# Kernel optimization log

Hardware: AMD Instinct MI355X
Metric: run time of the kernel (lower is better)

The kernel has to match this reference:

```python
import jax, jax.numpy as jnp
import numpy as np


def _l2norm(v, eps=1e-12):
    # torch F.normalize(dim=-1): v / clamp(||v||_2, min=eps)
    n = jnp.linalg.norm(v, axis=-1, keepdims=True)
    return v / jnp.maximum(n, eps)


def setup_inputs() -> dict:
    key = jax.random.key(0)
    ks = jax.random.split(key, 10)
    B, T, N, Ci, E, K, H = 64, 12, 1024, 64, 16, 3, 192
    O = H // 3  # subhidden size
    return {
        "x": jax.random.normal(ks[0], (B, N, Ci), jnp.float32),
        "x_window": jax.random.normal(ks[1], (B, T, N, 1), jnp.float32),
        "node_embeddings": jax.random.normal(ks[2], (N, E), jnp.float32) * 0.1,
        "ZPI": jax.random.normal(ks[3], (B, 3), jnp.float32),
        "supports_adj": jax.random.uniform(ks[4], (K, N, N), jnp.float32),
        "weights_pool": jax.random.normal(ks[5], (E, K, Ci, O), jnp.float32) * 0.1,
        "weights_pool_adj": jax.random.normal(ks[6], (E, K, Ci, O), jnp.float32) * 0.1,
        "weights_window": jax.random.normal(ks[7], (E, 1, O), jnp.float32) * 0.1,
        "bias_pool": jax.random.normal(ks[8], (E, H), jnp.float32) * 0.1,
        "T_param": jax.random.normal(ks[9], (T,), jnp.float32) * 0.1,
    }


def reference(x, x_window, node_embeddings, ZPI, supports_adj,
              weights_pool, weights_pool_adj, weights_window, bias_pool, T_param):
    N = node_embeddings.shape[0]
    K = weights_pool.shape[1]  # link_len

    # adaptive supports: softmax(relu(E E^T)) and its power series
    supports = jax.nn.softmax(jax.nn.relu(node_embeddings @ node_embeddings.T), axis=1)
    support_set = [jnp.eye(N, dtype=x.dtype), supports]
    for k in range(2, K):
        support_set.append(supports @ support_set[k - 1])
    S = jnp.stack(support_set, axis=0)  # (K, N, N)

    # per-node dynamic weights / bias
    weights = jnp.einsum('nd,dkio->nkio', node_embeddings, weights_pool)
    bias = node_embeddings @ bias_pool  # (N, H)

    # adaptive graph conv branch
    x_g = jnp.einsum('knm,bmc->bnkc', S, x)
    x_gconv = _l2norm(jnp.einsum('bnki,nkio->bno', x_g, weights))

    # static adjacency branch ('knn' repeated index = diagonal; sum over m --
    # faithful to the original torch einsum)
    weights_adj = jnp.einsum('nd,dkio->nkio', node_embeddings, weights_pool_adj)
    x_a = jnp.einsum('knn,bmc->bnkc', supports_adj, x)
    x_aconv = _l2norm(jnp.einsum('bnki,nkio->bno', x_a, weights_adj))

    # temporal window branch
    ww = jnp.einsum('nd,dio->nio', node_embeddings, weights_window)  # (N, 1, O)
    x_w = jnp.einsum('btni,nio->btno', x_window, ww)
    x_wconv = _l2norm(jnp.einsum('btno,t->bno', x_w, T_param))

    return jnp.concatenate([x_gconv, x_aconv, x_wconv], axis=-1) + bias
```

## Files before the change

kernel.cpp:

```cpp
#include <hip/hip_runtime.h>


typedef __attribute__((ext_vector_type(4))) float f32x4;
typedef __attribute__((ext_vector_type(8))) short short8;

#define DEVI static __device__ __forceinline__

DEVI short f2bf(float f) {
    unsigned int x = __builtin_bit_cast(unsigned int, f);
    x = (x + 0x7FFFu + ((x >> 16) & 1u)) >> 16;
    return (short)(unsigned short)x;
}
DEVI int swz(int row) { return ((row ^ (row >> 3)) & 7) << 3; }

DEVI f32x4 mfma16(short8 a, short8 b, f32x4 c) {
    return __builtin_amdgcn_mfma_f32_16x16x32_bf16(a, b, c, 0, 0, 0);
}

DEVI void gload16(const void* g, void* l) {
    __builtin_amdgcn_global_load_lds(
        (const __attribute__((address_space(1))) unsigned int*)g,
        (__attribute__((address_space(3))) unsigned int*)l, 16, 0, 0);
}

__global__ __launch_bounds__(256) void k_prep(
        const float* __restrict__ NE, const float* __restrict__ x,
        const float* __restrict__ xw, const float* __restrict__ adj,
        const float* __restrict__ wp, const float* __restrict__ wpa,
        const float* __restrict__ Tp,
        short* __restrict__ S, short* __restrict__ B2, short* __restrict__ A2,
        float* __restrict__ xsp, float* __restrict__ s_bn) {
    __shared__ float En[16];
    __shared__ float wsum[4];
    __shared__ float red[4][64];
    int bid = blockIdx.x, t = threadIdx.x;
    if (bid < 1024) {
        int n = bid;
        if (t < 16) En[t] = NE[n * 16 + t];
        __syncthreads();
        float e[4];
        float loc = 0.f;
#pragma unroll
        for (int i = 0; i < 4; ++i) {
            int m = t + 256 * i;
            const float* rp = NE + m * 16;
            float v = 0.f;
#pragma unroll
            for (int d = 0; d < 16; ++d) v += En[d] * rp[d];
            v = fmaxf(v, 0.f);
            e[i] = __expf(v);
            loc += e[i];
        }
#pragma unroll
        for (int off = 32; off; off >>= 1) loc += __shfl_xor(loc, off);
        if ((t & 63) == 0) wsum[t >> 6] = loc;
        __syncthreads();
        float inv = 1.f / (wsum[0] + wsum[1] + wsum[2] + wsum[3]);
#pragma unroll
        for (int i = 0; i < 4; ++i) S[n * 1024 + t + 256 * i] = f2bf(e[i] * inv);
        return;
    }
    int bid2 = bid - 1024;
    if (bid2 < 64) {
        int o = bid2, j = t;
        short row[64];
        if (j < 192) {
            int kk = j >> 6, i = j & 63;
#pragma unroll
            for (int d = 0; d < 16; ++d)
                row[d] = f2bf(wp[((d * 3 + kk) * 64 + i) * 64 + o]);
#pragma unroll
            for (int k = 16; k < 64; ++k) row[k] = 0;
        } else {
            int i2 = j - 192;
#pragma unroll
            for (int k = 0; k < 16; ++k) row[k] = 0;
#pragma unroll
            for (int d = 0; d < 16; ++d)
#pragma unroll
                for (int kk = 0; kk < 3; ++kk)
                    row[16 + d * 3 + kk] = f2bf(wpa[((d * 3 + kk) * 64 + i2) * 64 + o]);
        }
        short* dst = B2 + (o * 256 + j) * 64;
#pragma unroll
        for (int q = 0; q < 8; ++q) {
            short8 v;
#pragma unroll
            for (int e2 = 0; e2 < 8; ++e2) v[e2] = row[q * 8 + e2];
            *reinterpret_cast<short8*>(dst + q * 8) = v;
        }
    } else if (bid2 < 320) {
        int idx = bid2 - 64, b = idx >> 2, mq = idx & 3;
        int c = t & 63, q2 = t >> 6;
        int m0 = mq * 256 + q2 * 64;
        float s = 0.f;
        for (int mm = 0; mm < 64; ++mm) s += x[((size_t)b * 1024 + m0 + mm) * 64 + c];
        red[q2][c] = s;
        __syncthreads();
        if (t < 64) xsp[(b * 4 + mq) * 64 + t] = red[0][t] + red[1][t] + red[2][t] + red[3][t];
    } else if (bid2 < 336) {
        int idx = bid2 - 320;
        float tp[12];
#pragma unroll
        for (int i = 0; i < 12; ++i) tp[i] = Tp[i];
        for (int bb = 0; bb < 4; ++bb) {
            int b = idx * 4 + bb;
#pragma unroll
            for (int j2 = 0; j2 < 4; ++j2) {
                int nn = t + 256 * j2;
                float s = 0.f;
#pragma unroll
                for (int tt = 0; tt < 12; ++tt) s += xw[(b * 12 + tt) * 1024 + nn] * tp[tt];
                s_bn[b * 1024 + nn] = s;
            }
        }
    } else {
        int n = (bid2 - 336) * 256 + t;
        float Enr[16];
#pragma unroll
        for (int d = 0; d < 16; ++d) Enr[d] = NE[n * 16 + d];
        float dg[3];
#pragma unroll
        for (int k = 0; k < 3; ++k) dg[k] = adj[k * 1024 * 1024 + n * 1024 + n];
        short row[64];
#pragma unroll
        for (int d = 0; d < 16; ++d) row[d] = f2bf(Enr[d]);
#pragma unroll
        for (int d = 0; d < 16; ++d)
#pragma unroll
            for (int k = 0; k < 3; ++k) row[16 + d * 3 + k] = f2bf(Enr[d] * dg[k]);
        short* dst = A2 + n * 64;
#pragma unroll
        for (int q = 0; q < 8; ++q) {
            short8 v;
#pragma unroll
            for (int e2 = 0; e2 < 8; ++e2) v[e2] = row[q * 8 + e2];
            *reinterpret_cast<short8*>(dst + q * 8) = v;
        }
    }
}

__global__ __launch_bounds__(256) void k_mid(
        const short* __restrict__ S, const float* __restrict__ x,
        const short* __restrict__ A2, const short* __restrict__ B2,
        const float* __restrict__ xsp,
        short* __restrict__ Y1, short* __restrict__ Wall,
        short* __restrict__ xs_bf) {
    __shared__ __align__(16) short lds[16384];
    int bid = blockIdx.x, t = threadIdx.x;
    if (bid >= 1536) {
        int by = bid - 1536;
#pragma unroll
        for (int p = 0; p < 2; ++p) {
            int j = by * 512 + p * 256 + t;
            int b = j >> 6, c = j & 63;
            float s = xsp[(b * 4 + 0) * 64 + c] + xsp[(b * 4 + 1) * 64 + c] +
                      xsp[(b * 4 + 2) * 64 + c] + xsp[(b * 4 + 3) * 64 + c];
            xs_bf[j] = f2bf(s);
        }
        return;
    }
    short* As = lds;
    short* Bs = lds + 8192;
    int wid = t >> 6, lane = t & 63;
    int rsub = lane >> 3, csub = (lane & 7) * 8;
    int wm = wid & 1, wn = wid >> 1;
    int lr = lane & 15, lg = lane >> 4;
    if (bid < 512) {
        int bx = bid & 7, b = bid >> 3;
        const short* A = S + (size_t)bx * 131072;
        const float* xb = x + (size_t)b * 65536;
        int bm = t >> 2, bc = (t & 3) * 16;
        f32x4 acc[4][2] = {};
        for (int kt = 0; kt < 16; ++kt) {
#pragma unroll
            for (int q = 0; q < 4; ++q) {
                int row = q * 32 + wid * 8;
                gload16(A + (size_t)(row + rsub) * 1024 + kt * 64 + csub, As + row * 64);
            }
#pragma unroll
            for (int j = 0; j < 4; ++j) {
                float4 f = *reinterpret_cast<const float4*>(&xb[(kt * 64 + bm) * 64 + bc + 4 * j]);
                float vv[4] = {f.x, f.y, f.z, f.w};
#pragma unroll
                for (int e = 0; e < 4; ++e) {
                    int c = bc + 4 * j + e;
                    Bs[c * 64 + (bm ^ swz(c))] = f2bf(vv[e]);
                }
            }
            __syncthreads();
#pragma unroll
            for (int ks = 0; ks < 2; ++ks) {
                int kk = ks * 32 + lg * 8;
                short8 af[4], bfr[2];
#pragma unroll
                for (int i = 0; i < 4; ++i)
                    af[i] = *reinterpret_cast<const short8*>(&As[(wm * 64 + i * 16 + lr) * 64 + kk]);
#pragma unroll
                for (int nf = 0; nf < 2; ++nf) {
                    int c = wn * 32 + nf * 16 + lr;
                    bfr[nf] = *reinterpret_cast<const short8*>(&Bs[c * 64 + (kk ^ swz(c))]);
                }
#pragma unroll
                for (int i = 0; i < 4; ++i)
#pragma unroll
                    for (int nf = 0; nf < 2; ++nf)
                        acc[i][nf] = mfma16(af[i], bfr[nf], acc[i][nf]);
            }
            __syncthreads();
        }
#pragma unroll
        for (int i = 0; i < 4; ++i)
#pragma unroll
            for (int nf = 0; nf < 2; ++nf)
#pragma unroll
                for (int r = 0; r < 4; ++r) {
                    int g = wm * 64 + i * 16 + lg * 4 + r;
                    int c = wn * 32 + nf * 16 + lr;
                    Y1[((size_t)b * 1024 + bx * 128 + g) * 64 + c] = f2bf(acc[i][nf][r]);
                }
    } else {
        int idx = bid - 512, bx = idx & 127, by = idx >> 7;
#pragma unroll
        for (int i = 0; i < 4; ++i) {
            int slot = t + 256 * i;
            int row = slot >> 3, k8 = slot & 7;
            int sw = swz(row);
            short8 va = *reinterpret_cast<const short8*>(A2 + (by * 128 + row) * 64 + k8 * 8);
            *reinterpret_cast<short8*>(&As[row * 64 + ((k8 * 8) ^ sw)]) = va;
            short8 vb = *reinterpret_cast<const short8*>(B2 + (bx * 128 + row) * 64 + k8 * 8);
            *reinterpret_cast<short8*>(&Bs[row * 64 + ((k8 * 8) ^ sw)]) = vb;
        }
        __syncthreads();
        f32x4 acc[4][4] = {};
#pragma unroll
        for (int ks = 0; ks < 2; ++ks) {
            int kk = ks * 32 + lg * 8;
            short8 af[4], bfr[4];
#pragma unroll
            for (int mf = 0; mf < 4; ++mf) {
                int row = wm * 64 + mf * 16 + lr;
                af[mf] = *reinterpret_cast<const short8*>(&As[row * 64 + (kk ^ swz(row))]);
            }
#pragma unroll
            for (int nf = 0; nf < 4; ++nf) {
                int row = wn * 64 + nf * 16 + lr;
                bfr[nf] = *reinterpret_cast<const short8*>(&Bs[row * 64 + (kk ^ swz(row))]);
            }
#pragma unroll
            for (int mf = 0; mf < 4; ++mf)
#pragma unroll
                for (int nf = 0; nf < 4; ++nf)
                    acc[mf][nf] = mfma16(af[mf], bfr[nf], acc[mf][nf]);
        }
#pragma unroll
        for (int mf = 0; mf < 4; ++mf)
#pragma unroll
            for (int nf = 0; nf < 4; ++nf)
#pragma unroll
                for (int r = 0; r < 4; ++r) {
                    int row = by * 128 + wm * 64 + mf * 16 + lg * 4 + r;
                    int col = bx * 128 + wn * 64 + nf * 16 + lr;
                    int o = col >> 8, j = col & 255;
                    Wall[(size_t)row * 16384 + (size_t)(j >> 3) * 512 + o * 8 + (j & 7)] =
                        f2bf(acc[mf][nf][r]);
                }
    }
}

__global__ __launch_bounds__(256) void k_gemm2(const short* __restrict__ S,
                                               const short* __restrict__ Y1,
                                               short* __restrict__ Y2) {
    __shared__ __align__(16) short As[128 * 64];
    __shared__ __align__(16) short Bs[64 * 64];
    int bx = blockIdx.x & 7, b = blockIdx.x >> 3, t = threadIdx.x;
    int wid = t >> 6, lane = t & 63;
    int rsub = lane >> 3, csub = (lane & 7) * 8;
    int wm = wid & 1, wn = wid >> 1;
    int lr = lane & 15, lg = lane >> 4;
    const short* A = S + (size_t)bx * 131072;
    const short* Bh = Y1 + (size_t)b * 65536;
    int bc0 = (t & 7) * 8, bm = t >> 3;
    f32x4 acc[4][2] = {};
    for (int kt = 0; kt < 16; ++kt) {
#pragma unroll
        for (int q = 0; q < 4; ++q) {
            int row = q * 32 + wid * 8;
            gload16(A + (size_t)(row + rsub) * 1024 + kt * 64 + csub, As + row * 64);
        }
#pragma unroll
        for (int it = 0; it < 2; ++it) {
            int m = bm + 32 * it;
            short8 hv = *reinterpret_cast<const short8*>(&Bh[(kt * 64 + m) * 64 + bc0]);
#pragma unroll
            for (int j = 0; j < 8; ++j) {
                int c = bc0 + j;
                Bs[c * 64 + (m ^ swz(c))] = hv[j];
            }
        }
        __syncthreads();
#pragma unroll
        for (int ks = 0; ks < 2; ++ks) {
            int kk = ks * 32 + lg * 8;
            short8 af[4], bfr[2];
#pragma unroll
            for (int i = 0; i < 4; ++i)
                af[i] = *reinterpret_cast<const short8*>(&As[(wm * 64 + i * 16 + lr) * 64 + kk]);
#pragma unroll
            for (int nf = 0; nf < 2; ++nf) {
                int c = wn * 32 + nf * 16 + lr;
                bfr[nf] = *reinterpret_cast<const short8*>(&Bs[c * 64 + (kk ^ swz(c))]);
            }
#pragma unroll
            for (int i = 0; i < 4; ++i)
#pragma unroll
                for (int nf = 0; nf < 2; ++nf)
                    acc[i][nf] = mfma16(af[i], bfr[nf], acc[i][nf]);
        }
        __syncthreads();
    }
#pragma unroll
    for (int i = 0; i < 4; ++i)
#pragma unroll
        for (int nf = 0; nf < 2; ++nf)
#pragma unroll
            for (int r = 0; r < 4; ++r) {
                int g = wm * 64 + i * 16 + lg * 4 + r;
                int c = wn * 32 + nf * 16 + lr;
                Y2[((size_t)b * 1024 + bx * 128 + g) * 64 + c] = f2bf(acc[i][nf][r]);
            }
}

__global__ __launch_bounds__(256) void k_epi(
        const float* __restrict__ x, const short* __restrict__ Y1,
        const short* __restrict__ Y2, const short* __restrict__ xs_bf,
        const float* __restrict__ s_bn, const short* __restrict__ Wall,
        const float* __restrict__ NE, const float* __restrict__ bp,
        const float* __restrict__ wwin, float* __restrict__ out) {
    int n = blockIdx.x, t = threadIdx.x;
    __shared__ float E_l[16];
    __shared__ float bias_l[192];
    __shared__ float ww_l[64];
    __shared__ float sq_l[2][2][64];
    __shared__ float wwn_l;
    if (t < 16) E_l[t] = NE[n * 16 + t];
    int w = t >> 6, l = t & 63;
    int wm = w & 1, wn = w >> 1;
    int lr = l & 15, lg = l >> 4;
    short8 wfk[8][2];
#pragma unroll
    for (int ks = 0; ks < 8; ++ks)
#pragma unroll
        for (int nf = 0; nf < 2; ++nf) {
            int o = wn * 32 + nf * 16 + lr;
            wfk[ks][nf] = *reinterpret_cast<const short8*>(
                &Wall[(size_t)n * 16384 + (size_t)(ks * 4 + lg) * 512 + o * 8]);
        }
    short8 af[8][2];
#pragma unroll
    for (int ks = 0; ks < 8; ++ks)
#pragma unroll
        for (int mf = 0; mf < 2; ++mf) {
            int b = wm * 32 + mf * 16 + lr;
            int k0 = ks * 32 + lg * 8;
            if (ks < 2) {
                const float4* p =
                    reinterpret_cast<const float4*>(&x[((size_t)b * 1024 + n) * 64 + k0]);
                float4 p0 = p[0], p1 = p[1];
                short8 v;
                v[0] = f2bf(p0.x); v[1] = f2bf(p0.y); v[2] = f2bf(p0.z); v[3] = f2bf(p0.w);
                v[4] = f2bf(p1.x); v[5] = f2bf(p1.y); v[6] = f2bf(p1.z); v[7] = f2bf(p1.w);
                af[ks][mf] = v;
            } else if (ks < 4) {
                af[ks][mf] = *reinterpret_cast<const short8*>(
                    &Y1[((size_t)b * 1024 + n) * 64 + (k0 - 64)]);
            } else if (ks < 6) {
                af[ks][mf] = *reinterpret_cast<const short8*>(
                    &Y2[((size_t)b * 1024 + n) * 64 + (k0 - 128)]);
            } else {
                af[ks][mf] = *reinterpret_cast<const short8*>(&xs_bf[b * 64 + (k0 - 192)]);
            }
        }
    __syncthreads();
    if (t < 192) {
        float s = 0.f;
#pragma unroll
        for (int d = 0; d < 16; ++d) s += E_l[d] * bp[d * 192 + t];
        bias_l[t] = s;
    } else {
        int o = t - 192;
        float s = 0.f;
#pragma unroll
        for (int d = 0; d < 16; ++d) s += E_l[d] * wwin[d * 64 + o];
        ww_l[o] = s;
    }
    __syncthreads();
    if (t < 64) {
        float v = ww_l[t];
        float s2 = v * v;
#pragma unroll
        for (int off = 32; off; off >>= 1) s2 += __shfl_xor(s2, off);
        if (t == 0) wwn_l = sqrtf(s2);
    }
    f32x4 accg[2][2] = {};
    f32x4 acca[2][2] = {};
#pragma unroll
    for (int ks = 0; ks < 8; ++ks)
#pragma unroll
        for (int mf = 0; mf < 2; ++mf)
#pragma unroll
            for (int nf = 0; nf < 2; ++nf) {
                if (ks < 6) accg[mf][nf] = mfma16(af[ks][mf], wfk[ks][nf], accg[mf][nf]);
                else        acca[mf][nf] = mfma16(af[ks][mf], wfk[ks][nf], acca[mf][nf]);
            }
#pragma unroll
    for (int mf = 0; mf < 2; ++mf)
#pragma unroll
        for (int r = 0; r < 4; ++r) {
            float sg = accg[mf][0][r] * accg[mf][0][r] + accg[mf][1][r] * accg[mf][1][r];
            float sa = acca[mf][0][r] * acca[mf][0][r] + acca[mf][1][r] * acca[mf][1][r];
#pragma unroll
            for (int off = 1; off < 16; off <<= 1) {
                sg += __shfl_xor(sg, off);
                sa += __shfl_xor(sa, off);
            }
            if (lr == 0) {
                int b = wm * 32 + mf * 16 + lg * 4 + r;
                sq_l[0][wn][b] = sg;
                sq_l[1][wn][b] = sa;
            }
        }
    __syncthreads();
#pragma unroll
    for (int mf = 0; mf < 2; ++mf)
#pragma unroll
        for (int r = 0; r < 4; ++r) {
            int b = wm * 32 + mf * 16 + lg * 4 + r;
            float ig = 1.f / fmaxf(sqrtf(sq_l[0][0][b] + sq_l[0][1][b]), 1e-12f);
            float ia = 1.f / fmaxf(sqrtf(sq_l[1][0][b] + sq_l[1][1][b]), 1e-12f);
            float* po = out + ((size_t)b * 1024 + n) * 192;
#pragma unroll
            for (int nf = 0; nf < 2; ++nf) {
                int o = wn * 32 + nf * 16 + lr;
                po[o]      = accg[mf][nf][r] * ig + bias_l[o];
                po[64 + o] = acca[mf][nf][r] * ia + bias_l[64 + o];
            }
        }
    float wwn = wwn_l;
#pragma unroll
    for (int it = 0; it < 16; ++it) {
        int b = it * 4 + (t >> 6);
        int o = t & 63;
        float s = s_bn[b * 1024 + n];
        float pre = s * ww_l[o];
        float nrm = fabsf(s) * wwn;
        out[((size_t)b * 1024 + n) * 192 + 128 + o] = pre / fmaxf(nrm, 1e-12f) + bias_l[128 + o];
    }
}

extern "C" void kernel_launch(void* const* d_in, const int* in_sizes, int n_in,
                              void* d_out, int out_size, void* d_ws, size_t ws_size,
                              hipStream_t stream) {
    const float* x    = (const float*)d_in[0];
    const float* xw   = (const float*)d_in[1];
    const float* NE   = (const float*)d_in[2];
    const float* adj  = (const float*)d_in[4];
    const float* wp   = (const float*)d_in[5];
    const float* wpa  = (const float*)d_in[6];
    const float* wwin = (const float*)d_in[7];
    const float* bp   = (const float*)d_in[8];
    const float* Tp   = (const float*)d_in[9];
    float* out = (float*)d_out;

    char* ws = (char*)d_ws;
    const size_t OFF_S    = 0;
    const size_t OFF_Y1   = 2097152;
    const size_t OFF_Y2   = 10485760;
    const size_t OFF_WALL = 18874368;
    const size_t OFF_A2   = 52428800;
    const size_t OFF_B2   = 52559872;
    const size_t OFF_XSP  = 54657024;
    const size_t OFF_XSBF = 54722560;
    const size_t OFF_SBN  = 54730752;
    const size_t NEED     = 54992896;
    if (ws_size < NEED) return;

    short* S     = (short*)(ws + OFF_S);
    short* Y1    = (short*)(ws + OFF_Y1);
    short* Y2    = (short*)(ws + OFF_Y2);
    short* Wall  = (short*)(ws + OFF_WALL);
    short* A2    = (short*)(ws + OFF_A2);
    short* B2    = (short*)(ws + OFF_B2);
    float* xsp   = (float*)(ws + OFF_XSP);
    short* xs_bf = (short*)(ws + OFF_XSBF);
    float* s_bn  = (float*)(ws + OFF_SBN);

    k_prep<<<1364, 256, 0, stream>>>(NE, x, xw, adj, wp, wpa, Tp, S, B2, A2, xsp, s_bn);
    k_mid<<<1544, 256, 0, stream>>>(S, x, A2, B2, xsp, Y1, Wall, xs_bf);
    k_gemm2<<<512, 256, 0, stream>>>(S, Y1, Y2);
    k_epi<<<1024, 256, 0, stream>>>(x, Y1, Y2, xs_bf, s_bn, Wall, NE, bp, wwin, out);
}
```

Baseline: 126.8 us.

## Split fused prep/mid kernels and store Y1/Y2 node-major for epilogue

Splits the multi-role k_prep and k_mid kernels into separate kernels (supports softmax, small prep, gemm1, gemm2, weight gemm). Y1/Y2 move from batch-major to node-major layout, so the per-node epilogue reads contiguous rows. The epilogue now stages xs_bf in swizzled LDS and loads weight fragments per k-step instead of preloading all of them, which lowers register pressure. In exchange there are more kernel launches and less overlap between heterogeneous work that used to share one grid.

```diff
diff --git a/kernel.cpp b/kernel.cpp
--- a/kernel.cpp
+++ b/kernel.cpp
@@ -23,46 +23,46 @@
         (__attribute__((address_space(3))) unsigned int*)l, 16, 0, 0);
 }
 
-__global__ __launch_bounds__(256) void k_prep(
-        const float* __restrict__ NE, const float* __restrict__ x,
-        const float* __restrict__ xw, const float* __restrict__ adj,
+__global__ __launch_bounds__(256) void k_supports(const float* __restrict__ NE,
+                                                  short* __restrict__ S) {
+    int n = blockIdx.x, t = threadIdx.x;
+    __shared__ float En[16];
+    __shared__ float wsum[4];
+    if (t < 16) En[t] = NE[n * 16 + t];
+    __syncthreads();
+    float e[4];
+    float loc = 0.f;
+#pragma unroll
+    for (int i = 0; i < 4; ++i) {
+        int m = t + 256 * i;
+        const float* rp = NE + m * 16;
+        float v = 0.f;
+#pragma unroll
+        for (int d = 0; d < 16; ++d) v += En[d] * rp[d];
+        v = fmaxf(v, 0.f);
+        e[i] = __expf(v);
+        loc += e[i];
+    }
+#pragma unroll
+    for (int off = 32; off; off >>= 1) loc += __shfl_xor(loc, off);
+    if ((t & 63) == 0) wsum[t >> 6] = loc;
+    __syncthreads();
+    float inv = 1.f / (wsum[0] + wsum[1] + wsum[2] + wsum[3]);
+#pragma unroll
+    for (int i = 0; i < 4; ++i) S[n * 1024 + t + 256 * i] = f2bf(e[i] * inv);
+}
+
+__global__ __launch_bounds__(256) void k_small(
+        const float* __restrict__ x, const float* __restrict__ xw,
+        const float* __restrict__ NE, const float* __restrict__ adj,
         const float* __restrict__ wp, const float* __restrict__ wpa,
         const float* __restrict__ Tp,
-        short* __restrict__ S, short* __restrict__ B2, short* __restrict__ A2,
+        short* __restrict__ B2, short* __restrict__ A2,
         float* __restrict__ xsp, float* __restrict__ s_bn) {
-    __shared__ float En[16];
-    __shared__ float wsum[4];
     __shared__ float red[4][64];
     int bid = blockIdx.x, t = threadIdx.x;
-    if (bid < 1024) {
-        int n = bid;
-        if (t < 16) En[t] = NE[n * 16 + t];
-        __syncthreads();
-        float e[4];
-        float loc = 0.f;
-#pragma unroll
-        for (int i = 0; i < 4; ++i) {
-            int m = t + 256 * i;
-            const float* rp = NE + m * 16;
-            float v = 0.f;
-#pragma unroll
-            for (int d = 0; d < 16; ++d) v += En[d] * rp[d];
-            v = fmaxf(v, 0.f);
-            e[i] = __expf(v);
-            loc += e[i];
-        }
-#pragma unroll
-        for (int off = 32; off; off >>= 1) loc += __shfl_xor(loc, off);
-        if ((t & 63) == 0) wsum[t >> 6] = loc;
-        __syncthreads();
-        float inv = 1.f / (wsum[0] + wsum[1] + wsum[2] + wsum[3]);
-#pragma unroll
-        for (int i = 0; i < 4; ++i) S[n * 1024 + t + 256 * i] = f2bf(e[i] * inv);
-        return;
-    }
-    int bid2 = bid - 1024;
-    if (bid2 < 64) {
-        int o = bid2, j = t;
+    if (bid < 64) {
+        int o = bid, j = t;
         short row[64];
         if (j < 192) {
             int kk = j >> 6, i = j & 63;
@@ -89,8 +89,8 @@
             for (int e2 = 0; e2 < 8; ++e2) v[e2] = row[q * 8 + e2];
             *reinterpret_cast<short8*>(dst + q * 8) = v;
         }
-    } else if (bid2 < 320) {
-        int idx = bid2 - 64, b = idx >> 2, mq = idx & 3;
+    } else if (bid < 320) {
+        int idx = bid - 64, b = idx >> 2, mq = idx & 3;
         int c = t & 63, q2 = t >> 6;
         int m0 = mq * 256 + q2 * 64;
         float s = 0.f;
@@ -98,8 +98,8 @@
         red[q2][c] = s;
         __syncthreads();
         if (t < 64) xsp[(b * 4 + mq) * 64 + t] = red[0][t] + red[1][t] + red[2][t] + red[3][t];
-    } else if (bid2 < 336) {
-        int idx = bid2 - 320;
+    } else if (bid < 336) {
+        int idx = bid - 320;
         float tp[12];
 #pragma unroll
         for (int i = 0; i < 12; ++i) tp[i] = Tp[i];
@@ -115,20 +115,20 @@
             }
         }
     } else {
-        int n = (bid2 - 336) * 256 + t;
-        float Enr[16];
-#pragma unroll
-        for (int d = 0; d < 16; ++d) Enr[d] = NE[n * 16 + d];
+        int n = (bid - 336) * 256 + t;
+        float En[16];
+#pragma unroll
+        for (int d = 0; d < 16; ++d) En[d] = NE[n * 16 + d];
         float dg[3];
 #pragma unroll
         for (int k = 0; k < 3; ++k) dg[k] = adj[k * 1024 * 1024 + n * 1024 + n];
         short row[64];
 #pragma unroll
-        for (int d = 0; d < 16; ++d) row[d] = f2bf(Enr[d]);
+        for (int d = 0; d < 16; ++d) row[d] = f2bf(En[d]);
 #pragma unroll
         for (int d = 0; d < 16; ++d)
 #pragma unroll
-            for (int k = 0; k < 3; ++k) row[16 + d * 3 + k] = f2bf(Enr[d] * dg[k]);
+            for (int k = 0; k < 3; ++k) row[16 + d * 3 + k] = f2bf(En[d] * dg[k]);
         short* dst = A2 + n * 64;
 #pragma unroll
         for (int q = 0; q < 8; ++q) {
@@ -140,16 +140,139 @@
     }
 }
 
-__global__ __launch_bounds__(256) void k_mid(
-        const short* __restrict__ S, const float* __restrict__ x,
-        const short* __restrict__ A2, const short* __restrict__ B2,
-        const float* __restrict__ xsp,
-        short* __restrict__ Y1, short* __restrict__ Wall,
-        short* __restrict__ xs_bf) {
-    __shared__ __align__(16) short lds[16384];
-    int bid = blockIdx.x, t = threadIdx.x;
-    if (bid >= 1536) {
-        int by = bid - 1536;
+__global__ __launch_bounds__(256) void k_gemm1(const short* __restrict__ S,
+                                               const float* __restrict__ x,
+                                               short* __restrict__ Y1) {
+    __shared__ __align__(16) short As[128 * 64];
+    __shared__ __align__(16) short Bs[64 * 64];
+    int bx = blockIdx.x, b = blockIdx.y, t = threadIdx.x;
+    int wid = t >> 6, lane = t & 63;
+    int rsub = lane >> 3, csub = (lane & 7) * 8;
+    int wm = wid & 1, wn = wid >> 1;
+    int lr = lane & 15, lg = lane >> 4;
+    const short* A = S + (size_t)bx * 131072;
+    const float* xb = x + (size_t)b * 65536;
+    int bm = t >> 2, bc = (t & 3) * 16;
+    f32x4 acc[4][2] = {};
+    for (int kt = 0; kt < 16; ++kt) {
+#pragma unroll
+        for (int q = 0; q < 4; ++q) {
+            int row = q * 32 + wid * 8;
+            gload16(A + (size_t)(row + rsub) * 1024 + kt * 64 + csub, As + row * 64);
+        }
+#pragma unroll
+        for (int j = 0; j < 4; ++j) {
+            float4 f = *reinterpret_cast<const float4*>(&xb[(kt * 64 + bm) * 64 + bc + 4 * j]);
+            float vv[4] = {f.x, f.y, f.z, f.w};
+#pragma unroll
+            for (int e = 0; e < 4; ++e) {
+                int c = bc + 4 * j + e;
+                Bs[c * 64 + (bm ^ swz(c))] = f2bf(vv[e]);
+            }
+        }
+        __syncthreads();
+#pragma unroll
+        for (int ks = 0; ks < 2; ++ks) {
+            int kk = ks * 32 + lg * 8;
+            short8 af[4], bfr[2];
+#pragma unroll
+            for (int i = 0; i < 4; ++i)
+                af[i] = *reinterpret_cast<const short8*>(&As[(wm * 64 + i * 16 + lr) * 64 + kk]);
+#pragma unroll
+            for (int nf = 0; nf < 2; ++nf) {
+                int c = wn * 32 + nf * 16 + lr;
+                bfr[nf] = *reinterpret_cast<const short8*>(&Bs[c * 64 + (kk ^ swz(c))]);
+            }
+#pragma unroll
+            for (int i = 0; i < 4; ++i)
+#pragma unroll
+                for (int nf = 0; nf < 2; ++nf)
+                    acc[i][nf] = mfma16(af[i], bfr[nf], acc[i][nf]);
+        }
+        __syncthreads();
+    }
+#pragma unroll
+    for (int i = 0; i < 4; ++i)
+#pragma unroll
+        for (int nf = 0; nf < 2; ++nf)
+#pragma unroll
+            for (int r = 0; r < 4; ++r) {
+                int g = wm * 64 + i * 16 + lg * 4 + r;
+                int c = wn * 32 + nf * 16 + lr;
+                Y1[(size_t)(bx * 128 + g) * 4096 + b * 64 + c] = f2bf(acc[i][nf][r]);
+            }
+}
+
+__global__ __launch_bounds__(256) void k_gemm2(const short* __restrict__ S,
+                                               const short* __restrict__ Y1,
+                                               short* __restrict__ Y2) {
+    __shared__ __align__(16) short As[128 * 64];
+    __shared__ __align__(16) short Bs[64 * 64];
+    int bx = blockIdx.x, b = blockIdx.y, t = threadIdx.x;
+    int wid = t >> 6, lane = t & 63;
+    int rsub = lane >> 3, csub = (lane & 7) * 8;
+    int wm = wid & 1, wn = wid >> 1;
+    int lr = lane & 15, lg = lane >> 4;
+    const short* A = S + (size_t)bx * 131072;
+    int bm = t >> 3, bc0 = (t & 7) * 8;
+    f32x4 acc[4][2] = {};
+    for (int kt = 0; kt < 16; ++kt) {
+#pragma unroll
+        for (int q = 0; q < 4; ++q) {
+            int row = q * 32 + wid * 8;
+            gload16(A + (size_t)(row + rsub) * 1024 + kt * 64 + csub, As + row * 64);
+        }
+#pragma unroll
+        for (int it = 0; it < 2; ++it) {
+            int m = bm + 32 * it;
+            short8 hv = *reinterpret_cast<const short8*>(
+                &Y1[(size_t)(kt * 64 + m) * 4096 + b * 64 + bc0]);
+#pragma unroll
+            for (int j = 0; j < 8; ++j) {
+                int c = bc0 + j;
+                Bs[c * 64 + (m ^ swz(c))] = hv[j];
+            }
+        }
+        __syncthreads();
+#pragma unroll
+        for (int ks = 0; ks < 2; ++ks) {
+            int kk = ks * 32 + lg * 8;
+            short8 af[4], bfr[2];
+#pragma unroll
+            for (int i = 0; i < 4; ++i)
+                af[i] = *reinterpret_cast<const short8*>(&As[(wm * 64 + i * 16 + lr) * 64 + kk]);
+#pragma unroll
+            for (int nf = 0; nf < 2; ++nf) {
+                int c = wn * 32 + nf * 16 + lr;
+                bfr[nf] = *reinterpret_cast<const short8*>(&Bs[c * 64 + (kk ^ swz(c))]);
+            }
+#pragma unroll
+            for (int i = 0; i < 4; ++i)
+#pragma unroll
+                for (int nf = 0; nf < 2; ++nf)
+                    acc[i][nf] = mfma16(af[i], bfr[nf], acc[i][nf]);
+        }
+        __syncthreads();
+    }
+#pragma unroll
+    for (int i = 0; i < 4; ++i)
+#pragma unroll
+        for (int nf = 0; nf < 2; ++nf)
+#pragma unroll
+            for (int r = 0; r < 4; ++r) {
+                int g = wm * 64 + i * 16 + lg * 4 + r;
+                int c = wn * 32 + nf * 16 + lr;
+                Y2[(size_t)(bx * 128 + g) * 4096 + b * 64 + c] = f2bf(acc[i][nf][r]);
+            }
+}
+
+__global__ __launch_bounds__(256) void k_gemm_w(const short* __restrict__ A2,
+                                                const short* __restrict__ B2,
+                                                short* __restrict__ Wall,
+                                                const float* __restrict__ xsp,
+                                                short* __restrict__ xs_bf) {
+    int bx = blockIdx.x, by = blockIdx.y, t = threadIdx.x;
+    if (bx == 128) {
 #pragma unroll
         for (int p = 0; p < 2; ++p) {
             int j = by * 512 + p * 256 + t;
@@ -160,174 +283,54 @@
         }
         return;
     }
-    short* As = lds;
-    short* Bs = lds + 8192;
-    int wid = t >> 6, lane = t & 63;
-    int rsub = lane >> 3, csub = (lane & 7) * 8;
-    int wm = wid & 1, wn = wid >> 1;
-    int lr = lane & 15, lg = lane >> 4;
-    if (bid < 512) {
-        int bx = bid & 7, b = bid >> 3;
-        const short* A = S + (size_t)bx * 131072;
-        const float* xb = x + (size_t)b * 65536;
-        int bm = t >> 2, bc = (t & 3) * 16;
-        f32x4 acc[4][2] = {};
-        for (int kt = 0; kt < 16; ++kt) {
-#pragma unroll
-            for (int q = 0; q < 4; ++q) {
-                int row = q * 32 + wid * 8;
-                gload16(A + (size_t)(row + rsub) * 1024 + kt * 64 + csub, As + row * 64);
-            }
-#pragma unroll
-            for (int j = 0; j < 4; ++j) {
-                float4 f = *reinterpret_cast<const float4*>(&xb[(kt * 64 + bm) * 64 + bc + 4 * j]);
-                float vv[4] = {f.x, f.y, f.z, f.w};
-#pragma unroll
-                for (int e = 0; e < 4; ++e) {
-                    int c = bc + 4 * j + e;
-                    Bs[c * 64 + (bm ^ swz(c))] = f2bf(vv[e]);
-                }
-            }
-            __syncthreads();
-#pragma unroll
-            for (int ks = 0; ks < 2; ++ks) {
-                int kk = ks * 32 + lg * 8;
-                short8 af[4], bfr[2];
-#pragma unroll
-                for (int i = 0; i < 4; ++i)
-                    af[i] = *reinterpret_cast<const short8*>(&As[(wm * 64 + i * 16 + lr) * 64 + kk]);
-#pragma unroll
-                for (int nf = 0; nf < 2; ++nf) {
-                    int c = wn * 32 + nf * 16 + lr;
-                    bfr[nf] = *reinterpret_cast<const short8*>(&Bs[c * 64 + (kk ^ swz(c))]);
-                }
-#pragma unroll
-                for (int i = 0; i < 4; ++i)
-#pragma unroll
-                    for (int nf = 0; nf < 2; ++nf)
-                        acc[i][nf] = mfma16(af[i], bfr[nf], acc[i][nf]);
-            }
-            __syncthreads();
-        }
-#pragma unroll
-        for (int i = 0; i < 4; ++i)
-#pragma unroll
-            for (int nf = 0; nf < 2; ++nf)
-#pragma unroll
-                for (int r = 0; r < 4; ++r) {
-                    int g = wm * 64 + i * 16 + lg * 4 + r;
-                    int c = wn * 32 + nf * 16 + lr;
-                    Y1[((size_t)b * 1024 + bx * 128 + g) * 64 + c] = f2bf(acc[i][nf][r]);
-                }
-    } else {
-        int idx = bid - 512, bx = idx & 127, by = idx >> 7;
-#pragma unroll
-        for (int i = 0; i < 4; ++i) {
-            int slot = t + 256 * i;
-            int row = slot >> 3, k8 = slot & 7;
-            int sw = swz(row);
-            short8 va = *reinterpret_cast<const short8*>(A2 + (by * 128 + row) * 64 + k8 * 8);
-            *reinterpret_cast<short8*>(&As[row * 64 + ((k8 * 8) ^ sw)]) = va;
-            short8 vb = *reinterpret_cast<const short8*>(B2 + (bx * 128 + row) * 64 + k8 * 8);
-            *reinterpret_cast<short8*>(&Bs[row * 64 + ((k8 * 8) ^ sw)]) = vb;
-        }
-        __syncthreads();
-        f32x4 acc[4][4] = {};
-#pragma unroll
-        for (int ks = 0; ks < 2; ++ks) {
-            int kk = ks * 32 + lg * 8;
-            short8 af[4], bfr[4];
-#pragma unroll
-            for (int mf = 0; mf < 4; ++mf) {
-                int row = wm * 64 + mf * 16 + lr;
-                af[mf] = *reinterpret_cast<const short8*>(&As[row * 64 + (kk ^ swz(row))]);
-            }
-#pragma unroll
-            for (int nf = 0; nf < 4; ++nf) {
-                int row = wn * 64 + nf * 16 + lr;
-                bfr[nf] = *reinterpret_cast<const short8*>(&Bs[row * 64 + (kk ^ swz(row))]);
-            }
-#pragma unroll
-            for (int mf = 0; mf < 4; ++mf)
-#pragma unroll
-                for (int nf = 0; nf < 4; ++nf)
-                    acc[mf][nf] = mfma16(af[mf], bfr[nf], acc[mf][nf]);
+    __shared__ __align__(16) short As[128 * 64];
+    __shared__ __align__(16) short Bs[128 * 64];
+#pragma unroll
+    for (int i = 0; i < 4; ++i) {
+        int slot = t + 256 * i;
+        int row = slot >> 3, k8 = slot & 7;
+        int sw = swz(row);
+        short8 va = *reinterpret_cast<const short8*>(A2 + (by * 128 + row) * 64 + k8 * 8);
+        *reinterpret_cast<short8*>(&As[row * 64 + ((k8 * 8) ^ sw)]) = va;
+        short8 vb = *reinterpret_cast<const short8*>(B2 + (bx * 128 + row) * 64 + k8 * 8);
+        *reinterpret_cast<short8*>(&Bs[row * 64 + ((k8 * 8) ^ sw)]) = vb;
+    }
+    __syncthreads();
+    int w = t >> 6, l = t & 63;
+    int wm = w & 1, wn = w >> 1;
+    int lr = l & 15, lg = l >> 4;
+    f32x4 acc[4][4] = {};
+#pragma unroll
+    for (int ks = 0; ks < 2; ++ks) {
+        int kk = ks * 32 + lg * 8;
+        short8 af[4], bfr[4];
+#pragma unroll
+        for (int mf = 0; mf < 4; ++mf) {
+            int row = wm * 64 + mf * 16 + lr;
+            af[mf] = *reinterpret_cast<const short8*>(&As[row * 64 + (kk ^ swz(row))]);
+        }
+#pragma unroll
+        for (int nf = 0; nf < 4; ++nf) {
+            int row = wn * 64 + nf * 16 + lr;
+            bfr[nf] = *reinterpret_cast<const short8*>(&Bs[row * 64 + (kk ^ swz(row))]);
         }
 #pragma unroll
         for (int mf = 0; mf < 4; ++mf)
 #pragma unroll
             for (int nf = 0; nf < 4; ++nf)
-#pragma unroll
-                for (int r = 0; r < 4; ++r) {
-                    int row = by * 128 + wm * 64 + mf * 16 + lg * 4 + r;
-                    int col = bx * 128 + wn * 64 + nf * 16 + lr;
-                    int o = col >> 8, j = col & 255;
-                    Wall[(size_t)row * 16384 + (size_t)(j >> 3) * 512 + o * 8 + (j & 7)] =
-                        f2bf(acc[mf][nf][r]);
-                }
-    }
-}
-
-__global__ __launch_bounds__(256) void k_gemm2(const short* __restrict__ S,
-                                               const short* __restrict__ Y1,
-                                               short* __restrict__ Y2) {
-    __shared__ __align__(16) short As[128 * 64];
-    __shared__ __align__(16) short Bs[64 * 64];
-    int bx = blockIdx.x & 7, b = blockIdx.x >> 3, t = threadIdx.x;
-    int wid = t >> 6, lane = t & 63;
-    int rsub = lane >> 3, csub = (lane & 7) * 8;
-    int wm = wid & 1, wn = wid >> 1;
-    int lr = lane & 15, lg = lane >> 4;
-    const short* A = S + (size_t)bx * 131072;
-    const short* Bh = Y1 + (size_t)b * 65536;
-    int bc0 = (t & 7) * 8, bm = t >> 3;
-    f32x4 acc[4][2] = {};
-    for (int kt = 0; kt < 16; ++kt) {
-#pragma unroll
-        for (int q = 0; q < 4; ++q) {
-            int row = q * 32 + wid * 8;
-            gload16(A + (size_t)(row + rsub) * 1024 + kt * 64 + csub, As + row * 64);
-        }
-#pragma unroll
-        for (int it = 0; it < 2; ++it) {
-            int m = bm + 32 * it;
-            short8 hv = *reinterpret_cast<const short8*>(&Bh[(kt * 64 + m) * 64 + bc0]);
-#pragma unroll
-            for (int j = 0; j < 8; ++j) {
-                int c = bc0 + j;
-                Bs[c * 64 + (m ^ swz(c))] = hv[j];
-            }
-        }
-        __syncthreads();
-#pragma unroll
-        for (int ks = 0; ks < 2; ++ks) {
-            int kk = ks * 32 + lg * 8;
-            short8 af[4], bfr[2];
-#pragma unroll
-            for (int i = 0; i < 4; ++i)
-                af[i] = *reinterpret_cast<const short8*>(&As[(wm * 64 + i * 16 + lr) * 64 + kk]);
-#pragma unroll
-            for (int nf = 0; nf < 2; ++nf) {
-                int c = wn * 32 + nf * 16 + lr;
-                bfr[nf] = *reinterpret_cast<const short8*>(&Bs[c * 64 + (kk ^ swz(c))]);
-            }
-#pragma unroll
-            for (int i = 0; i < 4; ++i)
-#pragma unroll
-                for (int nf = 0; nf < 2; ++nf)
-                    acc[i][nf] = mfma16(af[i], bfr[nf], acc[i][nf]);
-        }
-        __syncthreads();
-    }
-#pragma unroll
-    for (int i = 0; i < 4; ++i)
-#pragma unroll
-        for (int nf = 0; nf < 2; ++nf)
+                acc[mf][nf] = mfma16(af[mf], bfr[nf], acc[mf][nf]);
+    }
+#pragma unroll
+    for (int mf = 0; mf < 4; ++mf)
+#pragma unroll
+        for (int nf = 0; nf < 4; ++nf)
 #pragma unroll
             for (int r = 0; r < 4; ++r) {
-                int g = wm * 64 + i * 16 + lg * 4 + r;
-                int c = wn * 32 + nf * 16 + lr;
-                Y2[((size_t)b * 1024 + bx * 128 + g) * 64 + c] = f2bf(acc[i][nf][r]);
+                int row = by * 128 + wm * 64 + mf * 16 + lg * 4 + r;
+                int col = bx * 128 + wn * 64 + nf * 16 + lr;
+                int o = col >> 8, j = col & 255;
+                Wall[(size_t)row * 16384 + (size_t)(j >> 3) * 512 + o * 8 + (j & 7)] =
+                    f2bf(acc[mf][nf][r]);
             }
 }
 
@@ -338,27 +341,49 @@
         const float* __restrict__ NE, const float* __restrict__ bp,
         const float* __restrict__ wwin, float* __restrict__ out) {
     int n = blockIdx.x, t = threadIdx.x;
+    __shared__ __align__(16) short xst[64 * 64];
     __shared__ float E_l[16];
     __shared__ float bias_l[192];
     __shared__ float ww_l[64];
     __shared__ float sq_l[2][2][64];
     __shared__ float wwn_l;
     if (t < 16) E_l[t] = NE[n * 16 + t];
+    __syncthreads();
+    if (t < 192) {
+        float s = 0.f;
+#pragma unroll
+        for (int d = 0; d < 16; ++d) s += E_l[d] * bp[d * 192 + t];
+        bias_l[t] = s;
+    } else {
+        int o = t - 192;
+        float s = 0.f;
+#pragma unroll
+        for (int d = 0; d < 16; ++d) s += E_l[d] * wwin[d * 64 + o];
+        ww_l[o] = s;
+    }
+#pragma unroll
+    for (int p = 0; p < 2; ++p) {
+        int idx = t + 256 * p;
+        int b = idx >> 3, q = idx & 7;
+        short8 v = *reinterpret_cast<const short8*>(&xs_bf[b * 64 + q * 8]);
+        *reinterpret_cast<short8*>(&xst[b * 64 + ((q * 8) ^ swz(b))]) = v;
+    }
+    __syncthreads();
+    if (t < 64) {
+        float v = ww_l[t];
+        float s2 = v * v;
+#pragma unroll
+        for (int off = 32; off; off >>= 1) s2 += __shfl_xor(s2, off);
+        if (t == 0) wwn_l = sqrtf(s2);
+    }
     int w = t >> 6, l = t & 63;
     int wm = w & 1, wn = w >> 1;
     int lr = l & 15, lg = l >> 4;
-    short8 wfk[8][2];
-#pragma unroll
-    for (int ks = 0; ks < 8; ++ks)
-#pragma unroll
-        for (int nf = 0; nf < 2; ++nf) {
-            int o = wn * 32 + nf * 16 + lr;
-            wfk[ks][nf] = *reinterpret_cast<const short8*>(
-                &Wall[(size_t)n * 16384 + (size_t)(ks * 4 + lg) * 512 + o * 8]);
-        }
-    short8 af[8][2];
-#pragma unroll
-    for (int ks = 0; ks < 8; ++ks)
+    f32x4 accg[2][2] = {};
+    f32x4 acca[2][2] = {};
+#pragma unroll
+    for (int ks = 0; ks < 8; ++ks) {
+        short8 af[2];
 #pragma unroll
         for (int mf = 0; mf < 2; ++mf) {
             int b = wm * 32 + mf * 16 + lr;
@@ -370,49 +395,33 @@
                 short8 v;
                 v[0] = f2bf(p0.x); v[1] = f2bf(p0.y); v[2] = f2bf(p0.z); v[3] = f2bf(p0.w);
                 v[4] = f2bf(p1.x); v[5] = f2bf(p1.y); v[6] = f2bf(p1.z); v[7] = f2bf(p1.w);
-                af[ks][mf] = v;
+                af[mf] = v;
             } else if (ks < 4) {
-                af[ks][mf] = *reinterpret_cast<const short8*>(
-                    &Y1[((size_t)b * 1024 + n) * 64 + (k0 - 64)]);
+                af[mf] = *reinterpret_cast<const short8*>(
+                    &Y1[(size_t)n * 4096 + b * 64 + (k0 - 64)]);
             } else if (ks < 6) {
-                af[ks][mf] = *reinterpret_cast<const short8*>(
-                    &Y2[((size_t)b * 1024 + n) * 64 + (k0 - 128)]);
+                af[mf] = *reinterpret_cast<const short8*>(
+                    &Y2[(size_t)n * 4096 + b * 64 + (k0 - 128)]);
             } else {
-                af[ks][mf] = *reinterpret_cast<const short8*>(&xs_bf[b * 64 + (k0 - 192)]);
-            }
-        }
-    __syncthreads();
-    if (t < 192) {
-        float s = 0.f;
-#pragma unroll
-        for (int d = 0; d < 16; ++d) s += E_l[d] * bp[d * 192 + t];
-        bias_l[t] = s;
-    } else {
-        int o = t - 192;
-        float s = 0.f;
-#pragma unroll
-        for (int d = 0; d < 16; ++d) s += E_l[d] * wwin[d * 64 + o];
-        ww_l[o] = s;
-    }
-    __syncthreads();
-    if (t < 64) {
-        float v = ww_l[t];
-        float s2 = v * v;
-#pragma unroll
-        for (int off = 32; off; off >>= 1) s2 += __shfl_xor(s2, off);
-        if (t == 0) wwn_l = sqrtf(s2);
-    }
-    f32x4 accg[2][2] = {};
-    f32x4 acca[2][2] = {};
-#pragma unroll
-    for (int ks = 0; ks < 8; ++ks)
+                af[mf] = *reinterpret_cast<const short8*>(
+                    &xst[b * 64 + ((k0 - 192) ^ swz(b))]);
+            }
+        }
+        short8 wfk[2];
+#pragma unroll
+        for (int nf = 0; nf < 2; ++nf) {
+            int o = wn * 32 + nf * 16 + lr;
+            wfk[nf] = *reinterpret_cast<const short8*>(
+                &Wall[(size_t)n * 16384 + (size_t)(ks * 4 + lg) * 512 + o * 8]);
+        }
 #pragma unroll
         for (int mf = 0; mf < 2; ++mf)
 #pragma unroll
             for (int nf = 0; nf < 2; ++nf) {
-                if (ks < 6) accg[mf][nf] = mfma16(af[ks][mf], wfk[ks][nf], accg[mf][nf]);
-                else        acca[mf][nf] = mfma16(af[ks][mf], wfk[ks][nf], acca[mf][nf]);
-            }
+                if (ks < 6) accg[mf][nf] = mfma16(af[mf], wfk[nf], accg[mf][nf]);
+                else        acca[mf][nf] = mfma16(af[mf], wfk[nf], acca[mf][nf]);
+            }
+    }
 #pragma unroll
     for (int mf = 0; mf < 2; ++mf)
 #pragma unroll
@@ -495,8 +504,10 @@
     short* xs_bf = (short*)(ws + OFF_XSBF);
     float* s_bn  = (float*)(ws + OFF_SBN);
 
-    k_prep<<<1364, 256, 0, stream>>>(NE, x, xw, adj, wp, wpa, Tp, S, B2, A2, xsp, s_bn);
-    k_mid<<<1544, 256, 0, stream>>>(S, x, A2, B2, xsp, Y1, Wall, xs_bf);
-    k_gemm2<<<512, 256, 0, stream>>>(S, Y1, Y2);
+    k_supports<<<1024, 256, 0, stream>>>(NE, S);
+    k_small<<<340, 256, 0, stream>>>(x, xw, NE, adj, wp, wpa, Tp, B2, A2, xsp, s_bn);
+    k_gemm1<<<dim3(8, 64), 256, 0, stream>>>(S, x, Y1);
+    k_gemm2<<<dim3(8, 64), 256, 0, stream>>>(S, Y1, Y2);
+    k_gemm_w<<<dim3(129, 8), 256, 0, stream>>>(A2, B2, Wall, xsp, xs_bf);
     k_epi<<<1024, 256, 0, stream>>>(x, Y1, Y2, xs_bf, s_bn, Wall, NE, bp, wwin, out);
 }
```

New measurement: 123.8 us. 2.4% less time.
